# Optimization experiments

Measured on AMD Instinct MI355X. Metric: run time of the kernel, lower is better.

## Reference

```python
import jax, jax.numpy as jnp
import numpy as np
import math

H = 16
D_MODEL = 1024
D_K = D_MODEL // H
B = 4
S = 2048


def setup_inputs() -> dict:
    key = jax.random.key(0)
    ks = jax.random.split(key, 11)
    s_in = 1.0 / math.sqrt(D_MODEL)
    inp = {
        "query": jax.random.normal(ks[0], (B, S, D_MODEL), dtype=jnp.float32),
        "key_": jax.random.normal(ks[1], (B, S, D_MODEL), dtype=jnp.float32),
        "value": jax.random.normal(ks[2], (B, S, D_MODEL), dtype=jnp.float32),
        # stacked per-head projection weights: [h, d_model, d_k]
        "Wq": jax.random.uniform(ks[3], (H, D_MODEL, D_K), jnp.float32, -s_in, s_in),
        "bq": jax.random.uniform(ks[4], (H, D_K), jnp.float32, -s_in, s_in),
        "Wk": jax.random.uniform(ks[5], (H, D_MODEL, D_K), jnp.float32, -s_in, s_in),
        "bk": jax.random.uniform(ks[6], (H, D_K), jnp.float32, -s_in, s_in),
        "Wv": jax.random.uniform(ks[7], (H, D_MODEL, D_K), jnp.float32, -s_in, s_in),
        "bv": jax.random.uniform(ks[8], (H, D_K), jnp.float32, -s_in, s_in),
        "Wo": jax.random.uniform(ks[9], (D_MODEL, D_MODEL), jnp.float32, -s_in, s_in),
        "bo": jax.random.uniform(ks[10], (D_MODEL,), jnp.float32, -s_in, s_in),
    }
    return inp


def reference(query, key_, value, Wq, bq, Wk, bk, Wv, bv, Wo, bo):
    # Per-head projections, batched over heads: [b,s,m] x [h,m,k] -> [b,h,s,k]
    q = jnp.einsum("bsm,hmk->bhsk", query, Wq) + bq[None, :, None, :]
    k = jnp.einsum("bsm,hmk->bhsk", key_, Wk) + bk[None, :, None, :]
    v = jnp.einsum("bsm,hmk->bhsk", value, Wv) + bv[None, :, None, :]
    # scores: q @ k^T -> [b,h,Sq,Sk]
    scores = jnp.einsum("bhqk,bhsk->bhqs", q, k) / jnp.sqrt(jnp.float32(D_K))
    # NOTE: original code softmaxes over dim=1 of the per-head [N,Sq,Sk]
    # tensor, i.e. the QUERY axis (axis=2 here). Mask has no effect
    # (masked_fill result is discarded in the source), so it is omitted.
    attn = jax.nn.softmax(scores, axis=2)
    ctx = jnp.einsum("bhqs,bhsk->bhqk", attn, v)  # [b,h,Sq,d_k]
    # concat heads along last dim (head-major order matches torch.cat)
    ctx = jnp.transpose(ctx, (0, 2, 1, 3)).reshape(B, S, D_MODEL)
    out = ctx @ Wo.T + bo  # final_W; dropout = identity (eval mode)
    return out
```

## Files before the change

kernel.cpp:

```cpp
#include <hip/hip_runtime.h>


#define DEV __device__ __forceinline__

typedef __bf16 bf16x8 __attribute__((ext_vector_type(8)));
typedef float  f32x4  __attribute__((ext_vector_type(4)));

DEV unsigned short f2bf(float f) {
    __bf16 h = (__bf16)f;
    return __builtin_bit_cast(unsigned short, h);
}

DEV bf16x8 ldfrag(const unsigned short* p) {
    return *reinterpret_cast<const bf16x8*>(p);
}

DEV float fast_exp2(float x) {
#if __has_builtin(__builtin_amdgcn_exp2f)
    return __builtin_amdgcn_exp2f(x);
#else
    return exp2f(x);
#endif
}

DEV void cvt8_store(unsigned short* dst, float4 a, float4 b) {
    bf16x8 v;
    v[0]=(__bf16)a.x; v[1]=(__bf16)a.y; v[2]=(__bf16)a.z; v[3]=(__bf16)a.w;
    v[4]=(__bf16)b.x; v[5]=(__bf16)b.y; v[6]=(__bf16)b.z; v[7]=(__bf16)b.w;
    *reinterpret_cast<bf16x8*>(dst) = v;
}

#define MFMA(a,b,c) __builtin_amdgcn_mfma_f32_16x16x32_bf16((a),(b),(c),0,0,0)

#define QSCALE 0.18033688011112042f

__global__ __launch_bounds__(256) void wprep(const float* __restrict__ Wq,
                                             const float* __restrict__ Wk,
                                             const float* __restrict__ Wv,
                                             const float* __restrict__ Wo,
                                             unsigned short* __restrict__ Wt,
                                             unsigned short* __restrict__ Wot) {
    int idx = blockIdx.x * 256 + threadIdx.x;
    int which = blockIdx.y;
    if (which == 3) { Wot[idx] = f2bf(Wo[idx]); return; }
    const float* W = (which == 0) ? Wq : (which == 1) ? Wk : Wv;
    int n = idx >> 10, m = idx & 1023;
    int h = n >> 6, k = n & 63;
    Wt[(size_t)which * 1048576 + idx] = f2bf(W[h * 65536 + m * 64 + k]);
}

__global__ __launch_bounds__(256) void proj_gemm(
        const float* __restrict__ Xq, const float* __restrict__ Xk,
        const float* __restrict__ Xv, const unsigned short* __restrict__ Wt,
        const float* __restrict__ bq, const float* __restrict__ bk,
        const float* __restrict__ bv,
        unsigned short* __restrict__ Qh, unsigned short* __restrict__ Kh,
        unsigned short* __restrict__ Vt) {
    const int tid = threadIdx.x;
    const int bm = blockIdx.x, bn = blockIdx.y, z = blockIdx.z;
    const float* X = (z == 0) ? Xq : (z == 1) ? Xk : Xv;
    const unsigned short* Bt = Wt + (size_t)z * 1048576;
    const float* bias = (z == 0) ? bq : (z == 1) ? bk : bv;

    __shared__ __align__(16) unsigned short As[128 * 40];
    __shared__ __align__(16) unsigned short Bs[128 * 40];

    const int lane = tid & 63, wid = tid >> 6;
    const int l16 = lane & 15, quad = lane >> 4;
    const int wm = wid & 1, wn = wid >> 1;

    f32x4 acc[4][4] = {};

    for (int kt = 0; kt < 32; ++kt) {
        __syncthreads();
        const int k0 = kt * 32;
#pragma unroll
        for (int i = 0; i < 2; ++i) {
            int seg = tid + i * 256;
            int row = seg >> 2, s4 = seg & 3;
            const float* gp = X + (size_t)(bm * 128 + row) * 1024 + k0 + s4 * 8;
            float4 f0 = *(const float4*)gp;
            float4 f1 = *(const float4*)(gp + 4);
            cvt8_store(&As[row * 40 + s4 * 8], f0, f1);
            const unsigned short* bp = Bt + (size_t)(bn * 128 + row) * 1024 + k0 + s4 * 8;
            *(uint4*)&Bs[row * 40 + s4 * 8] = *(const uint4*)bp;
        }
        __syncthreads();
        bf16x8 af[4], bfr[4];
#pragma unroll
        for (int mi = 0; mi < 4; ++mi)
            af[mi] = ldfrag(&As[(wm * 64 + mi * 16 + l16) * 40 + quad * 8]);
#pragma unroll
        for (int ni = 0; ni < 4; ++ni)
            bfr[ni] = ldfrag(&Bs[(wn * 64 + ni * 16 + l16) * 40 + quad * 8]);
#pragma unroll
        for (int mi = 0; mi < 4; ++mi)
#pragma unroll
            for (int ni = 0; ni < 4; ++ni)
                acc[mi][ni] = MFMA(af[mi], bfr[ni], acc[mi][ni]);
    }

#pragma unroll
    for (int mi = 0; mi < 4; ++mi)
#pragma unroll
        for (int ni = 0; ni < 4; ++ni)
#pragma unroll
            for (int r = 0; r < 4; ++r) {
                int row = bm * 128 + wm * 64 + mi * 16 + quad * 4 + r;
                int col = bn * 128 + wn * 64 + ni * 16 + l16;
                float v = acc[mi][ni][r] + bias[col];
                if (z == 0) v *= QSCALE;
                int b = row >> 11, s = row & 2047;
                int h = col >> 6, k = col & 63;
                unsigned short o = f2bf(v);
                if (z == 2) {
                    Vt[(size_t)((b * 16 + h) * 64 + k) * 2048 + s] = o;
                } else {
                    unsigned short* O = (z == 0) ? Qh : Kh;
                    O[(size_t)((b * 16 + h) * 2048 + s) * 64 + k] = o;
                }
            }
}

__global__ __launch_bounds__(256) void colsum(const unsigned short* __restrict__ Qh,
                                              const unsigned short* __restrict__ Kh,
                                              float* __restrict__ Dcol) {
    const int tid = threadIdx.x;
    const int st = blockIdx.x, bh = blockIdx.y;
    const unsigned short* Qb = Qh + (size_t)bh * 2048 * 64;
    const unsigned short* Kb = Kh + (size_t)bh * 2048 * 64;

    __shared__ __align__(16) unsigned short Qs[128 * 72];
    __shared__ float Dtmp[2][128];

    const int lane = tid & 63, wid = tid >> 6;
    const int l16 = lane & 15, quad = lane >> 4;
    const int wm = wid & 1, wn = wid >> 1;

    bf16x8 bfr[2][4];
#pragma unroll
    for (int ks = 0; ks < 2; ++ks)
#pragma unroll
        for (int ni = 0; ni < 4; ++ni)
            bfr[ks][ni] = ldfrag(&Kb[(size_t)(st * 128 + wn * 64 + ni * 16 + l16) * 64 +
                                     ks * 32 + quad * 8]);

    float psum[4] = {0.f, 0.f, 0.f, 0.f};
    for (int q0 = 0; q0 < 2048; q0 += 128) {
        __syncthreads();
#pragma unroll
        for (int i = 0; i < 4; ++i) {
            int seg = tid + i * 256;
            int row = seg >> 3, sc = seg & 7;
            *(uint4*)&Qs[row * 72 + sc * 8] =
                *(const uint4*)&Qb[(size_t)(q0 + row) * 64 + sc * 8];
        }
        __syncthreads();
        f32x4 acc[4][4] = {};
#pragma unroll
        for (int ks = 0; ks < 2; ++ks) {
            bf16x8 af[4];
#pragma unroll
            for (int mi = 0; mi < 4; ++mi)
                af[mi] = ldfrag(&Qs[(wm * 64 + mi * 16 + l16) * 72 + ks * 32 + quad * 8]);
#pragma unroll
            for (int mi = 0; mi < 4; ++mi)
#pragma unroll
                for (int ni = 0; ni < 4; ++ni)
                    acc[mi][ni] = MFMA(af[mi], bfr[ks][ni], acc[mi][ni]);
        }
#pragma unroll
        for (int ni = 0; ni < 4; ++ni) {
            float d = 0.f;
#pragma unroll
            for (int mi = 0; mi < 4; ++mi)
#pragma unroll
                for (int r = 0; r < 4; ++r)
                    d += fast_exp2(acc[mi][ni][r]);
            psum[ni] += d;
        }
    }
#pragma unroll
    for (int ni = 0; ni < 4; ++ni) {
        float v = psum[ni];
        v += __shfl_xor(v, 16, 64);
        v += __shfl_xor(v, 32, 64);
        if (quad == 0) Dtmp[wm][wn * 64 + ni * 16 + l16] = v;
    }
    __syncthreads();
    if (tid < 128)
        Dcol[(size_t)bh * 2048 + st * 128 + tid] = Dtmp[0][tid] + Dtmp[1][tid];
}

__global__ __launch_bounds__(256) void vscale(unsigned short* __restrict__ Vt,
                                              const float* __restrict__ Dcol) {
    const int k = blockIdx.x, bh = blockIdx.y, t = threadIdx.x;
    size_t base = ((size_t)bh * 64 + k) * 2048 + t * 8;
    bf16x8 v = *(const bf16x8*)&Vt[base];
    float4 d0 = *(const float4*)&Dcol[bh * 2048 + t * 8];
    float4 d1 = *(const float4*)&Dcol[bh * 2048 + t * 8 + 4];
    bf16x8 o;
    o[0] = (__bf16)((float)v[0] / d0.x);
    o[1] = (__bf16)((float)v[1] / d0.y);
    o[2] = (__bf16)((float)v[2] / d0.z);
    o[3] = (__bf16)((float)v[3] / d0.w);
    o[4] = (__bf16)((float)v[4] / d1.x);
    o[5] = (__bf16)((float)v[5] / d1.y);
    o[6] = (__bf16)((float)v[6] / d1.z);
    o[7] = (__bf16)((float)v[7] / d1.w);
    *(bf16x8*)&Vt[base] = o;
}

__global__ __launch_bounds__(256) void attnpv(const unsigned short* __restrict__ Qh,
                                              const unsigned short* __restrict__ Kh,
                                              const unsigned short* __restrict__ Vn,
                                              unsigned short* __restrict__ Ctx) {
    const int tid = threadIdx.x;
    const int qt = blockIdx.x, bh = blockIdx.y;
    const int b = bh >> 4, h = bh & 15;
    const unsigned short* Qb = Qh + (size_t)bh * 2048 * 64;
    const unsigned short* Kb = Kh + (size_t)bh * 2048 * 64;
    const unsigned short* Vb = Vn + (size_t)bh * 64 * 2048;

    __shared__ __align__(16) unsigned short Ks[64 * 72];
    __shared__ __align__(16) unsigned short Vs[64 * 72];
    __shared__ __align__(16) unsigned short Ps[128 * 72];

    const int lane = tid & 63, wid = tid >> 6;
    const int l16 = lane & 15, quad = lane >> 4;
    const int wm = wid & 1, wn = wid >> 1;

    bf16x8 af[2][4];
#pragma unroll
    for (int ks = 0; ks < 2; ++ks)
#pragma unroll
        for (int mi = 0; mi < 4; ++mi)
            af[ks][mi] = ldfrag(&Qb[(size_t)(qt * 128 + wm * 64 + mi * 16 + l16) * 64 +
                                    ks * 32 + quad * 8]);

    f32x4 cacc[2][4] = {};
    for (int s0 = 0; s0 < 2048; s0 += 64) {
        __syncthreads();
#pragma unroll
        for (int i = 0; i < 2; ++i) {
            int seg = tid + i * 256;
            int row = seg >> 3, sc = seg & 7;
            *(uint4*)&Ks[row * 72 + sc * 8] =
                *(const uint4*)&Kb[(size_t)(s0 + row) * 64 + sc * 8];
            *(uint4*)&Vs[row * 72 + sc * 8] =
                *(const uint4*)&Vb[(size_t)row * 2048 + s0 + sc * 8];
        }
        __syncthreads();

        f32x4 sacc[4][2] = {};
#pragma unroll
        for (int ks = 0; ks < 2; ++ks) {
            bf16x8 bfr[2];
#pragma unroll
            for (int nj = 0; nj < 2; ++nj)
                bfr[nj] = ldfrag(&Ks[(wn * 32 + nj * 16 + l16) * 72 + ks * 32 + quad * 8]);
#pragma unroll
            for (int mi = 0; mi < 4; ++mi)
#pragma unroll
                for (int nj = 0; nj < 2; ++nj)
                    sacc[mi][nj] = MFMA(af[ks][mi], bfr[nj], sacc[mi][nj]);
        }
#pragma unroll
        for (int mi = 0; mi < 4; ++mi)
#pragma unroll
            for (int nj = 0; nj < 2; ++nj) {
                int scol = wn * 32 + nj * 16 + l16;
#pragma unroll
                for (int r = 0; r < 4; ++r) {
                    int qrow = wm * 64 + mi * 16 + quad * 4 + r;
                    Ps[qrow * 72 + scol] = f2bf(fast_exp2(sacc[mi][nj][r]));
                }
            }
        __syncthreads();

#pragma unroll
        for (int ks2 = 0; ks2 < 2; ++ks2) {
            bf16x8 pa[2], vbf[4];
#pragma unroll
            for (int mi = 0; mi < 2; ++mi)
                pa[mi] = ldfrag(&Ps[(wid * 32 + mi * 16 + l16) * 72 + ks2 * 32 + quad * 8]);
#pragma unroll
            for (int ni = 0; ni < 4; ++ni)
                vbf[ni] = ldfrag(&Vs[(ni * 16 + l16) * 72 + ks2 * 32 + quad * 8]);
#pragma unroll
            for (int mi = 0; mi < 2; ++mi)
#pragma unroll
                for (int ni = 0; ni < 4; ++ni)
                    cacc[mi][ni] = MFMA(pa[mi], vbf[ni], cacc[mi][ni]);
        }
    }

#pragma unroll
    for (int mi = 0; mi < 2; ++mi)
#pragma unroll
        for (int ni = 0; ni < 4; ++ni)
#pragma unroll
            for (int r = 0; r < 4; ++r) {
                int q = qt * 128 + wid * 32 + mi * 16 + quad * 4 + r;
                int dk = ni * 16 + l16;
                Ctx[(size_t)(b * 2048 + q) * 1024 + h * 64 + dk] = f2bf(cacc[mi][ni][r]);
            }
}

__global__ __launch_bounds__(256) void out_gemm(const unsigned short* __restrict__ A,
                                                const unsigned short* __restrict__ Bt,
                                                const float* __restrict__ bias,
                                                float* __restrict__ Out) {
    const int tid = threadIdx.x;
    const int bm = blockIdx.x, bn = blockIdx.y;

    __shared__ __align__(16) unsigned short As[128 * 40];
    __shared__ __align__(16) unsigned short Bs[128 * 40];

    const int lane = tid & 63, wid = tid >> 6;
    const int l16 = lane & 15, quad = lane >> 4;
    const int wm = wid & 1, wn = wid >> 1;

    f32x4 acc[4][4] = {};
    for (int kt = 0; kt < 32; ++kt) {
        __syncthreads();
        const int k0 = kt * 32;
#pragma unroll
        for (int i = 0; i < 2; ++i) {
            int seg = tid + i * 256;
            int row = seg >> 2, s4 = seg & 3;
            *(uint4*)&As[row * 40 + s4 * 8] =
                *(const uint4*)&A[(size_t)(bm * 128 + row) * 1024 + k0 + s4 * 8];
            *(uint4*)&Bs[row * 40 + s4 * 8] =
                *(const uint4*)&Bt[(size_t)(bn * 128 + row) * 1024 + k0 + s4 * 8];
        }
        __syncthreads();
        bf16x8 af[4], bfr[4];
#pragma unroll
        for (int mi = 0; mi < 4; ++mi)
            af[mi] = ldfrag(&As[(wm * 64 + mi * 16 + l16) * 40 + quad * 8]);
#pragma unroll
        for (int ni = 0; ni < 4; ++ni)
            bfr[ni] = ldfrag(&Bs[(wn * 64 + ni * 16 + l16) * 40 + quad * 8]);
#pragma unroll
        for (int mi = 0; mi < 4; ++mi)
#pragma unroll
            for (int ni = 0; ni < 4; ++ni)
                acc[mi][ni] = MFMA(af[mi], bfr[ni], acc[mi][ni]);
    }
#pragma unroll
    for (int mi = 0; mi < 4; ++mi)
#pragma unroll
        for (int ni = 0; ni < 4; ++ni)
#pragma unroll
            for (int r = 0; r < 4; ++r) {
                int row = bm * 128 + wm * 64 + mi * 16 + quad * 4 + r;
                int col = bn * 128 + wn * 64 + ni * 16 + l16;
                Out[(size_t)row * 1024 + col] = acc[mi][ni][r] + bias[col];
            }
}

extern "C" void kernel_launch(void* const* d_in, const int* in_sizes, int n_in,
                              void* d_out, int out_size, void* d_ws, size_t ws_size,
                              hipStream_t stream) {
    (void)in_sizes; (void)n_in; (void)out_size; (void)ws_size;
    const float* query = (const float*)d_in[0];
    const float* key_  = (const float*)d_in[1];
    const float* value = (const float*)d_in[2];
    const float* Wq    = (const float*)d_in[3];
    const float* bq    = (const float*)d_in[4];
    const float* Wk    = (const float*)d_in[5];
    const float* bk    = (const float*)d_in[6];
    const float* Wv    = (const float*)d_in[7];
    const float* bv    = (const float*)d_in[8];
    const float* Wo    = (const float*)d_in[9];
    const float* bo    = (const float*)d_in[10];
    float* Out = (float*)d_out;

    char* ws = (char*)d_ws;
    const size_t MB = 1024 * 1024;
    unsigned short* Wt   = (unsigned short*)(ws);
    unsigned short* Wot  = (unsigned short*)(ws + 6 * MB);
    unsigned short* Qh   = (unsigned short*)(ws + 8 * MB);
    unsigned short* Kh   = (unsigned short*)(ws + 24 * MB);
    unsigned short* Vt   = (unsigned short*)(ws + 40 * MB);
    unsigned short* Ctx  = (unsigned short*)(ws + 56 * MB);
    float* Dcol          = (float*)(ws + 72 * MB);

    wprep<<<dim3(4096, 4), dim3(256), 0, stream>>>(Wq, Wk, Wv, Wo, Wt, Wot);
    proj_gemm<<<dim3(64, 8, 3), dim3(256), 0, stream>>>(query, key_, value, Wt,
                                                        bq, bk, bv, Qh, Kh, Vt);
    colsum<<<dim3(16, 64), dim3(256), 0, stream>>>(Qh, Kh, Dcol);
    vscale<<<dim3(64, 64), dim3(256), 0, stream>>>(Vt, Dcol);
    attnpv<<<dim3(16, 64), dim3(256), 0, stream>>>(Qh, Kh, Vt, Ctx);
    out_gemm<<<dim3(64, 8), dim3(256), 0, stream>>>(Ctx, Wot, bo, Out);
}
```

Baseline: 517.4 us.

## Load K/V/Q fragments directly from global and transpose MFMA roles in attention

The colsum kernel drops its shared-memory Q staging. Each wave now holds its own K rows in registers and streams Q fragments straight from global, with the reduction done by lane shuffles instead of shared memory. The attnpv kernel drops the shared K and V tiles and computes S^T and ctx^T with swapped MFMA operands. It loads K and V fragments directly from global and prefetches the next K tile, so only the P tile goes through shared memory, and it writes the context with vectorised 4-wide stores. This is meant to cut LDS traffic and barriers, at the cost of redundant global or L2 reads across waves.

```diff
diff --git a/kernel.cpp b/kernel.cpp
--- a/kernel.cpp
+++ b/kernel.cpp
@@ -130,66 +130,61 @@
     const unsigned short* Qb = Qh + (size_t)bh * 2048 * 64;
     const unsigned short* Kb = Kh + (size_t)bh * 2048 * 64;
 
-    __shared__ __align__(16) unsigned short Qs[128 * 72];
-    __shared__ float Dtmp[2][128];
-
     const int lane = tid & 63, wid = tid >> 6;
     const int l16 = lane & 15, quad = lane >> 4;
-    const int wm = wid & 1, wn = wid >> 1;
-
-    bf16x8 bfr[2][4];
-#pragma unroll
-    for (int ks = 0; ks < 2; ++ks)
-#pragma unroll
-        for (int ni = 0; ni < 4; ++ni)
-            bfr[ks][ni] = ldfrag(&Kb[(size_t)(st * 128 + wn * 64 + ni * 16 + l16) * 64 +
-                                     ks * 32 + quad * 8]);
-
-    float psum[4] = {0.f, 0.f, 0.f, 0.f};
-    for (int q0 = 0; q0 < 2048; q0 += 128) {
-        __syncthreads();
-#pragma unroll
-        for (int i = 0; i < 4; ++i) {
-            int seg = tid + i * 256;
-            int row = seg >> 3, sc = seg & 7;
-            *(uint4*)&Qs[row * 72 + sc * 8] =
-                *(const uint4*)&Qb[(size_t)(q0 + row) * 64 + sc * 8];
+
+    bf16x8 kf[2][2];
+#pragma unroll
+    for (int mi = 0; mi < 2; ++mi)
+#pragma unroll
+        for (int ks = 0; ks < 2; ++ks)
+            kf[mi][ks] = ldfrag(&Kb[(size_t)(st * 128 + wid * 32 + mi * 16 + l16) * 64 +
+                                    ks * 32 + quad * 8]);
+
+    float psum[2][4] = {};
+    const unsigned short* qp = Qb + (size_t)l16 * 64 + quad * 8;
+    for (int q0 = 0; q0 < 2048; q0 += 64) {
+        bf16x8 qf[2][4];
+#pragma unroll
+        for (int nj = 0; nj < 4; ++nj)
+#pragma unroll
+            for (int ks = 0; ks < 2; ++ks)
+                qf[ks][nj] = ldfrag(qp + (size_t)(q0 + nj * 16) * 64 + ks * 32);
+        f32x4 acc[2][4] = {};
+#pragma unroll
+        for (int ks = 0; ks < 2; ++ks)
+#pragma unroll
+            for (int mi = 0; mi < 2; ++mi)
+#pragma unroll
+                for (int nj = 0; nj < 4; ++nj)
+                    acc[mi][nj] = MFMA(kf[mi][ks], qf[ks][nj], acc[mi][nj]);
+#pragma unroll
+        for (int mi = 0; mi < 2; ++mi)
+#pragma unroll
+            for (int nj = 0; nj < 4; ++nj)
+#pragma unroll
+                for (int r = 0; r < 4; ++r)
+                    psum[mi][r] += fast_exp2(acc[mi][nj][r]);
+    }
+#pragma unroll
+    for (int mi = 0; mi < 2; ++mi)
+#pragma unroll
+        for (int r = 0; r < 4; ++r) {
+            float v = psum[mi][r];
+            v += __shfl_xor(v, 1, 64);
+            v += __shfl_xor(v, 2, 64);
+            v += __shfl_xor(v, 4, 64);
+            v += __shfl_xor(v, 8, 64);
+            psum[mi][r] = v;
         }
-        __syncthreads();
-        f32x4 acc[4][4] = {};
-#pragma unroll
-        for (int ks = 0; ks < 2; ++ks) {
-            bf16x8 af[4];
-#pragma unroll
-            for (int mi = 0; mi < 4; ++mi)
-                af[mi] = ldfrag(&Qs[(wm * 64 + mi * 16 + l16) * 72 + ks * 32 + quad * 8]);
-#pragma unroll
-            for (int mi = 0; mi < 4; ++mi)
-#pragma unroll
-                for (int ni = 0; ni < 4; ++ni)
-                    acc[mi][ni] = MFMA(af[mi], bfr[ks][ni], acc[mi][ni]);
-        }
-#pragma unroll
-        for (int ni = 0; ni < 4; ++ni) {
-            float d = 0.f;
-#pragma unroll
-            for (int mi = 0; mi < 4; ++mi)
-#pragma unroll
-                for (int r = 0; r < 4; ++r)
-                    d += fast_exp2(acc[mi][ni][r]);
-            psum[ni] += d;
-        }
+    if (l16 == 0) {
+#pragma unroll
+        for (int mi = 0; mi < 2; ++mi)
+#pragma unroll
+            for (int r = 0; r < 4; ++r)
+                Dcol[(size_t)bh * 2048 + st * 128 + wid * 32 + mi * 16 + quad * 4 + r] =
+                    psum[mi][r];
     }
-#pragma unroll
-    for (int ni = 0; ni < 4; ++ni) {
-        float v = psum[ni];
-        v += __shfl_xor(v, 16, 64);
-        v += __shfl_xor(v, 32, 64);
-        if (quad == 0) Dtmp[wm][wn * 64 + ni * 16 + l16] = v;
-    }
-    __syncthreads();
-    if (tid < 128)
-        Dcol[(size_t)bh * 2048 + st * 128 + tid] = Dtmp[0][tid] + Dtmp[1][tid];
 }
 
 __global__ __launch_bounds__(256) void vscale(unsigned short* __restrict__ Vt,
@@ -222,89 +217,98 @@
     const unsigned short* Kb = Kh + (size_t)bh * 2048 * 64;
     const unsigned short* Vb = Vn + (size_t)bh * 64 * 2048;
 
-    __shared__ __align__(16) unsigned short Ks[64 * 72];
-    __shared__ __align__(16) unsigned short Vs[64 * 72];
     __shared__ __align__(16) unsigned short Ps[128 * 72];
 
     const int lane = tid & 63, wid = tid >> 6;
     const int l16 = lane & 15, quad = lane >> 4;
-    const int wm = wid & 1, wn = wid >> 1;
-
-    bf16x8 af[2][4];
+    const int wq = wid & 1, ws = wid >> 1;
+
+    bf16x8 qf[2][4];
 #pragma unroll
     for (int ks = 0; ks < 2; ++ks)
 #pragma unroll
-        for (int mi = 0; mi < 4; ++mi)
-            af[ks][mi] = ldfrag(&Qb[(size_t)(qt * 128 + wm * 64 + mi * 16 + l16) * 64 +
+        for (int nj = 0; nj < 4; ++nj)
+            qf[ks][nj] = ldfrag(&Qb[(size_t)(qt * 128 + wq * 64 + nj * 16 + l16) * 64 +
                                     ks * 32 + quad * 8]);
+
+    const unsigned short* kp = Kb + (size_t)(ws * 32 + l16) * 64 + quad * 8;
+    const unsigned short* vp = Vb + (size_t)(ws * 32 + l16) * 2048 + quad * 8;
+    unsigned short* psw = &Ps[(size_t)(wq * 64 + l16) * 72 + ws * 32 + quad * 4];
+    const unsigned short* psr = &Ps[(size_t)(wq * 64 + l16) * 72 + quad * 8];
+
+    bf16x8 kf[2][2];
+#pragma unroll
+    for (int mi = 0; mi < 2; ++mi)
+#pragma unroll
+        for (int ks = 0; ks < 2; ++ks)
+            kf[mi][ks] = ldfrag(kp + mi * 1024 + ks * 32);
 
     f32x4 cacc[2][4] = {};
     for (int s0 = 0; s0 < 2048; s0 += 64) {
-        __syncthreads();
-#pragma unroll
-        for (int i = 0; i < 2; ++i) {
-            int seg = tid + i * 256;
-            int row = seg >> 3, sc = seg & 7;
-            *(uint4*)&Ks[row * 72 + sc * 8] =
-                *(const uint4*)&Kb[(size_t)(s0 + row) * 64 + sc * 8];
-            *(uint4*)&Vs[row * 72 + sc * 8] =
-                *(const uint4*)&Vb[(size_t)row * 2048 + s0 + sc * 8];
+        f32x4 sacc[2][4] = {};
+#pragma unroll
+        for (int ks = 0; ks < 2; ++ks)
+#pragma unroll
+            for (int mi = 0; mi < 2; ++mi)
+#pragma unroll
+                for (int nj = 0; nj < 4; ++nj)
+                    sacc[mi][nj] = MFMA(kf[mi][ks], qf[ks][nj], sacc[mi][nj]);
+
+        bf16x8 vf[2][2];
+#pragma unroll
+        for (int mi = 0; mi < 2; ++mi)
+#pragma unroll
+            for (int ks = 0; ks < 2; ++ks)
+                vf[mi][ks] = ldfrag(vp + (size_t)mi * 32768 + ks * 32 + s0);
+        const int s1 = (s0 + 64) & 2047;
+#pragma unroll
+        for (int mi = 0; mi < 2; ++mi)
+#pragma unroll
+            for (int ks = 0; ks < 2; ++ks)
+                kf[mi][ks] = ldfrag(kp + (size_t)s1 * 64 + mi * 1024 + ks * 32);
+
+#pragma unroll
+        for (int mi = 0; mi < 2; ++mi)
+#pragma unroll
+            for (int nj = 0; nj < 4; ++nj) {
+                ushort4 p;
+                p.x = f2bf(fast_exp2(sacc[mi][nj][0]));
+                p.y = f2bf(fast_exp2(sacc[mi][nj][1]));
+                p.z = f2bf(fast_exp2(sacc[mi][nj][2]));
+                p.w = f2bf(fast_exp2(sacc[mi][nj][3]));
+                *(ushort4*)(psw + (size_t)nj * 16 * 72 + mi * 16) = p;
+            }
+        __syncthreads();
+
+        bf16x8 pf[2][4];
+#pragma unroll
+        for (int ks2 = 0; ks2 < 2; ++ks2)
+#pragma unroll
+            for (int nj = 0; nj < 4; ++nj)
+                pf[ks2][nj] = ldfrag(psr + (size_t)nj * 16 * 72 + ks2 * 32);
+#pragma unroll
+        for (int ks2 = 0; ks2 < 2; ++ks2)
+#pragma unroll
+            for (int mi = 0; mi < 2; ++mi)
+#pragma unroll
+                for (int nj = 0; nj < 4; ++nj)
+                    cacc[mi][nj] = MFMA(vf[mi][ks2], pf[ks2][nj], cacc[mi][nj]);
+        __syncthreads();
+    }
+
+#pragma unroll
+    for (int mi = 0; mi < 2; ++mi)
+#pragma unroll
+        for (int nj = 0; nj < 4; ++nj) {
+            int q = qt * 128 + wq * 64 + nj * 16 + l16;
+            int k = ws * 32 + mi * 16 + quad * 4;
+            ushort4 o;
+            o.x = f2bf(cacc[mi][nj][0]);
+            o.y = f2bf(cacc[mi][nj][1]);
+            o.z = f2bf(cacc[mi][nj][2]);
+            o.w = f2bf(cacc[mi][nj][3]);
+            *(ushort4*)&Ctx[(size_t)(b * 2048 + q) * 1024 + h * 64 + k] = o;
         }
-        __syncthreads();
-
-        f32x4 sacc[4][2] = {};
-#pragma unroll
-        for (int ks = 0; ks < 2; ++ks) {
-            bf16x8 bfr[2];
-#pragma unroll
-            for (int nj = 0; nj < 2; ++nj)
-                bfr[nj] = ldfrag(&Ks[(wn * 32 + nj * 16 + l16) * 72 + ks * 32 + quad * 8]);
-#pragma unroll
-            for (int mi = 0; mi < 4; ++mi)
-#pragma unroll
-                for (int nj = 0; nj < 2; ++nj)
-                    sacc[mi][nj] = MFMA(af[ks][mi], bfr[nj], sacc[mi][nj]);
-        }
-#pragma unroll
-        for (int mi = 0; mi < 4; ++mi)
-#pragma unroll
-            for (int nj = 0; nj < 2; ++nj) {
-                int scol = wn * 32 + nj * 16 + l16;
-#pragma unroll
-                for (int r = 0; r < 4; ++r) {
-                    int qrow = wm * 64 + mi * 16 + quad * 4 + r;
-                    Ps[qrow * 72 + scol] = f2bf(fast_exp2(sacc[mi][nj][r]));
-                }
-            }
-        __syncthreads();
-
-#pragma unroll
-        for (int ks2 = 0; ks2 < 2; ++ks2) {
-            bf16x8 pa[2], vbf[4];
-#pragma unroll
-            for (int mi = 0; mi < 2; ++mi)
-                pa[mi] = ldfrag(&Ps[(wid * 32 + mi * 16 + l16) * 72 + ks2 * 32 + quad * 8]);
-#pragma unroll
-            for (int ni = 0; ni < 4; ++ni)
-                vbf[ni] = ldfrag(&Vs[(ni * 16 + l16) * 72 + ks2 * 32 + quad * 8]);
-#pragma unroll
-            for (int mi = 0; mi < 2; ++mi)
-#pragma unroll
-                for (int ni = 0; ni < 4; ++ni)
-                    cacc[mi][ni] = MFMA(pa[mi], vbf[ni], cacc[mi][ni]);
-        }
-    }
-
-#pragma unroll
-    for (int mi = 0; mi < 2; ++mi)
-#pragma unroll
-        for (int ni = 0; ni < 4; ++ni)
-#pragma unroll
-            for (int r = 0; r < 4; ++r) {
-                int q = qt * 128 + wid * 32 + mi * 16 + quad * 4 + r;
-                int dk = ni * 16 + l16;
-                Ctx[(size_t)(b * 2048 + q) * 1024 + h * 64 + dk] = f2bf(cacc[mi][ni][r]);
-            }
 }
 
 __global__ __launch_bounds__(256) void out_gemm(const unsigned short* __restrict__ A,
```

Measured after the change: 545.7 us. 5.5% more time.
